# Optimization experiments

Hardware: AMD Instinct MI355X
Metric: run time of the kernel (lower is better)

Reference implementation:

```python
import jax, jax.numpy as jnp
import numpy as np

B = 32768
D_IN = 512      # input_dim == dict_dim (forced by the STE add)
HID = 512       # hard-coded hidden width of linear1
D = 512         # dict_dim / embedding_dim
P = 8           # per_factor_dict_size: number of codebooks / MLP branches
K = 10          # num_factor: codebook size (rows per embedding table)
COMMIT = 0.25


def setup_inputs() -> dict:
    key = jax.random.key(0)
    ks = jax.random.split(key, 7)
    s1 = 1.0 / np.sqrt(D_IN)
    s2 = 1.0 / np.sqrt(HID)
    return {
        "inputs": jax.random.normal(ks[0], (B, D_IN), jnp.float32),
        "W1": jax.random.uniform(ks[1], (P, HID, D_IN), jnp.float32, -s1, s1),
        "b1": jax.random.uniform(ks[2], (P, HID), jnp.float32, -s1, s1),
        "W2": jax.random.uniform(ks[3], (P, D, HID), jnp.float32, -s2, s2),
        "b2": jax.random.uniform(ks[4], (P, D), jnp.float32, -s2, s2),
        # embedding init: uniform(-1/num_factor, 1/num_factor)
        "E": jax.random.uniform(ks[5], (P, K, D), jnp.float32, -1.0 / K, 1.0 / K),
        "label_gen": jax.random.randint(ks[6], (B,), 0, K, jnp.int64),
    }


def reference(inputs, W1, b1, W2, b2, E, label_gen):
    sg = jax.lax.stop_gradient
    # P parallel 2-layer MLPs: [P, B, D]
    h = jax.nn.relu(jnp.einsum("bd,phd->pbh", inputs, W1) + b1[:, None, :])
    z = jnp.einsum("pbh,peh->pbe", h, W2) + b2[:, None, :]
    # squared-distance expansion per codebook: [P, B, K]
    distances = (
        jnp.sum(z * z, axis=-1, keepdims=True)
        + jnp.sum(E * E, axis=-1)[:, None, :]
        - 2.0 * jnp.einsum("pbd,pkd->pbk", z, E)
    )
    ave_distances = jnp.mean(distances, axis=0)          # [B, K]
    idx = jnp.argmin(ave_distances, axis=1)              # [B]
    # one-hot @ E[p] then mean over p == mean codebook gathered at idx
    Emean = jnp.mean(E, axis=0)                          # [K, D]
    vq = Emean[idx]                                      # [B, D]
    vq_z = inputs + sg(vq - inputs)                      # straight-through
    # all_vq_z[j] = mean_p E[p, j]; losses vs every code row: [K, B]
    diff1 = Emean[:, None, :] - sg(inputs)[None, :, :]   # [K, B, D]
    diff2 = sg(Emean)[:, None, :] - inputs[None, :, :]
    all_vq_loss = jnp.sum(diff1 * diff1, axis=-1) + COMMIT * jnp.sum(diff2 * diff2, axis=-1)
    all_vq_z = inputs[None, :, :] + sg(Emean[:, None, :] - inputs[None, :, :])  # [K, B, D]
    changed_vq_z = Emean[label_gen]                      # [B, D]
    return (vq_z, distances, all_vq_z, all_vq_loss, changed_vq_z)
```

## Files before the change

### kernel.cpp

```cpp
#include <hip/hip_runtime.h>
#include <stdint.h>

typedef _Float16 f16;
typedef _Float16 f16x8 __attribute__((ext_vector_type(8)));
typedef float f32x4 __attribute__((ext_vector_type(4)));

#define B_ROWS 32768
#define DIM 512
#define NP 8
#define NK 10

typedef __attribute__((address_space(3))) unsigned int lds_u32;
typedef __attribute__((address_space(1))) const unsigned int gbl_u32;

__device__ __forceinline__ void gload_lds16(const void* g, void* l) {
  __builtin_amdgcn_global_load_lds((gbl_u32*)(uintptr_t)g, (lds_u32*)(uintptr_t)l, 16, 0, 0);
}


__global__ void split_kernel(const float* __restrict__ src, f16* __restrict__ hi,
                             f16* __restrict__ lo, int n) {
  int i = blockIdx.x * 256 + threadIdx.x;
  int stride = gridDim.x * 256;
  for (; i < n; i += stride) {
    float v = src[i];
    f16 h = (f16)v;
    hi[i] = h;
    lo[i] = (f16)(v - (float)h);
  }
}

__global__ void emean_kernel(const float* __restrict__ E, float* __restrict__ Emean) {
  int i = blockIdx.x * 256 + threadIdx.x;
  if (i < NK * DIM) {
    float s = 0.f;
#pragma unroll
    for (int p = 0; p < NP; ++p) s += E[p * NK * DIM + i];
    Emean[i] = s * 0.125f;
  }
}

__global__ void enorm_kernel(const float* __restrict__ E, const float* __restrict__ Emean,
                             float* __restrict__ E2, float* __restrict__ E2m) {
  int bid = blockIdx.x;
  const float* src = (bid < 80) ? (E + (size_t)bid * DIM) : (Emean + (size_t)(bid - 80) * DIM);
  int lane = threadIdx.x;
  float s = 0.f;
  for (int i = lane; i < DIM; i += 64) {
    float v = src[i];
    s = fmaf(v, v, s);
  }
#pragma unroll
  for (int m = 1; m < 64; m <<= 1) s += __shfl_xor(s, m, 64);
  if (lane == 0) {
    if (bid < 80) E2[bid] = s;
    else E2m[bid - 80] = s;
  }
}

__global__ __launch_bounds__(512) void etilde_kernel(const float* __restrict__ W2,
                                                     const float* __restrict__ b2,
                                                     const float* __restrict__ E,
                                                     float* __restrict__ Et,
                                                     float* __restrict__ c_) {
  const int p = blockIdx.x / NK, k = blockIdx.x % NK;
  const int h = threadIdx.x;
  __shared__ float Er[512];
  __shared__ float red[8];
  Er[h] = E[((size_t)p * NK + k) * DIM + h];
  __syncthreads();
  const float* Wp = W2 + (size_t)p * DIM * DIM;
  float s = 0.f;
#pragma unroll 8
  for (int d = 0; d < DIM; ++d) s = fmaf(Wp[(size_t)d * DIM + h], Er[d], s);
  Et[((size_t)p * NK + k) * DIM + h] = s;
  float t = b2[p * DIM + h] * Er[h];
#pragma unroll
  for (int m = 1; m < 64; m <<= 1) t += __shfl_xor(t, m, 64);
  if ((h & 63) == 0) red[h >> 6] = t;
  __syncthreads();
  if (h == 0) {
    float cc = 0.f;
#pragma unroll
    for (int i = 0; i < 8; ++i) cc += red[i];
    c_[p * NK + k] = cc;
  }
}

__global__ void epack_kernel(const float* __restrict__ Et, f16* __restrict__ EimgH,
                             f16* __restrict__ EimgL) {
  int i = blockIdx.x * 256 + threadIdx.x;
  const int tot = NP * 16 * 520;
  if (i >= tot) return;
  int p = i / (16 * 520);
  int rem = i % (16 * 520);
  int k = rem / 520, h = rem % 520;
  float v = (k < NK && h < DIM) ? Et[((size_t)p * NK + k) * DIM + h] : 0.f;
  f16 hi = (f16)v;
  EimgH[i] = hi;
  EimgL[i] = (f16)(v - (float)hi);
}


template <int EPI, int NBN, int NPROD, int GRP>
__global__ __launch_bounds__(256) void gemmA(
    const f16* __restrict__ Ah_, const f16* __restrict__ Al_, int lda, int apitch,
    const f16* __restrict__ Bh_, const f16* __restrict__ Bl_, int bpitch,
    const float* __restrict__ bias_, int bias_pitch,
    f16* __restrict__ Oh, f16* __restrict__ Ol, int ldo,
    float* __restrict__ part2) {
  __shared__ f16 smem[32768];
  const int tid = threadIdx.x;
  const int lane = tid & 63;
  const int wave = tid >> 6;
  const int wr = wave >> 1, wc = wave & 1;
  const int p = blockIdx.z;

  const int q8 = gridDim.x >> 3;
  const int bid = blockIdx.x;
  const int swz = (bid & 7) * q8 + (bid >> 3);
  const int band = swz / (GRP * NBN);
  const int r_ = swz % (GRP * NBN);
  const int bm = band * GRP + (r_ % GRP);
  const int bn = r_ / GRP;
  const int m0 = bm * 128, n0 = bn * 128;

  const f16* Ahp = Ah_ + (size_t)p * apitch;
  const f16* Alp = Al_ + (size_t)p * apitch;
  const f16* Bhp = Bh_ + (size_t)p * bpitch;
  const f16* Blp = Bl_ + (size_t)p * bpitch;

  const int NT = (NPROD == 3) ? 24 : 8;

  f32x4 acc[4][4] = {};

  auto stage = [&](int buf, int t) {
    const f16* As;
    const f16* Bs;
    int k0;
    if (NPROD == 3) {
      int pr = t % 3;
      As = (pr == 2) ? Alp : Ahp;
      Bs = (pr == 1) ? Blp : Bhp;
      k0 = (t / 3) * 64;
    } else {
      As = Ahp;
      Bs = Bhp;
      k0 = t * 64;
    }
    f16* sA = smem + buf * 16384;
    f16* sB = sA + 8192;
#pragma unroll
    for (int j = 0; j < 4; ++j) {
      int r = j * 32 + (tid >> 3);
      int c = ((tid & 7) ^ (r & 7)) * 8;
      gload_lds16(As + (size_t)(m0 + r) * lda + k0 + c, sA + j * 2048 + tid * 8);
      gload_lds16(Bs + (size_t)(n0 + r) * 512 + k0 + c, sB + j * 2048 + tid * 8);
    }
  };

  stage(0, 0);
  __syncthreads();

  const int g = lane >> 4, rl = lane & 15;

  for (int s = 0; s < NT; ++s) {
    int nx = s + 1;
    if (nx < NT) stage(nx & 1, nx);
    const char* sA = (const char*)(smem + (s & 1) * 16384);
    const char* sB = sA + 16384;
    f16x8 af[4][2], bf[4][2];
#pragma unroll
    for (int i = 0; i < 4; ++i) {
      int ra = wr * 64 + i * 16 + rl;
      int rb = wc * 64 + i * 16 + rl;
#pragma unroll
      for (int kk = 0; kk < 2; ++kk) {
        int cb = kk * 64 + g * 16;
        af[i][kk] = *(const f16x8*)(sA + ra * 128 + (cb ^ ((ra & 7) << 4)));
        bf[i][kk] = *(const f16x8*)(sB + rb * 128 + (cb ^ ((rb & 7) << 4)));
      }
    }
#pragma unroll
    for (int i = 0; i < 4; ++i)
#pragma unroll
      for (int jn = 0; jn < 4; ++jn)
#pragma unroll
        for (int kk = 0; kk < 2; ++kk)
          acc[i][jn] = __builtin_amdgcn_mfma_f32_16x16x32_f16(af[i][kk], bf[jn][kk], acc[i][jn], 0, 0, 0);
    __syncthreads();
  }

  if (EPI == 0) {
#pragma unroll
    for (int jn = 0; jn < 4; ++jn) {
      int cg = n0 + wc * 64 + jn * 16 + rl;
      float bv = bias_[cg];
#pragma unroll
      for (int i = 0; i < 4; ++i) {
        int r0 = m0 + wr * 64 + i * 16 + g * 4;
#pragma unroll
        for (int r = 0; r < 4; ++r) {
          float z = acc[i][jn][r] + bv;
          z = fmaxf(z, 0.f);
          f16 h = (f16)z;
          size_t off = (size_t)(r0 + r) * ldo + cg;
          Oh[off] = h;
          Ol[off] = (f16)(z - (float)h);
        }
      }
    }
  } else {
    const float* bp = bias_ + (size_t)p * bias_pitch;
    float bvals[4];
#pragma unroll
    for (int jn = 0; jn < 4; ++jn) bvals[jn] = bp[n0 + wc * 64 + jn * 16 + rl];
    const int ch = bn * 2 + wc;
    float* pb = part2 + (size_t)(p * 8 + ch) * B_ROWS;
#pragma unroll
    for (int i = 0; i < 4; ++i) {
#pragma unroll
      for (int r = 0; r < 4; ++r) {
        float q = 0.f;
#pragma unroll
        for (int jn = 0; jn < 4; ++jn) {
          float z = acc[i][jn][r] + bvals[jn];
          q = fmaf(z, z, q);
        }
#pragma unroll
        for (int m = 1; m < 16; m <<= 1) q += __shfl_xor(q, m, 64);
        if (rl == 0) pb[m0 + wr * 64 + i * 16 + g * 4 + r] = q;
      }
    }
  }
}


__global__ __launch_bounds__(256) void dots_mfma(const f16* __restrict__ Hh,
                                                 const f16* __restrict__ Hl,
                                                 const f16* __restrict__ EimgH,
                                                 const f16* __restrict__ EimgL,
                                                 const float* __restrict__ c_,
                                                 float* __restrict__ gout) {
  __shared__ f16 sH[8192];
  __shared__ f16 sL[8192];
  __shared__ f16 sEh[16 * 520];
  __shared__ f16 sEl[16 * 520];
  const int tid = threadIdx.x;
  const int lane = tid & 63, wave = tid >> 6;
  const int p = blockIdx.y;
  const int r0 = blockIdx.x * 128;
  {
    const uint32_t* ih = (const uint32_t*)(EimgH + (size_t)p * 16 * 520);
    const uint32_t* il = (const uint32_t*)(EimgL + (size_t)p * 16 * 520);
    uint32_t* oh = (uint32_t*)sEh;
    uint32_t* ol = (uint32_t*)sEl;
    for (int i = tid; i < 16 * 520 / 2; i += 256) {
      oh[i] = ih[i];
      ol[i] = il[i];
    }
  }
  const int gq = lane >> 4, rl = lane & 15;
  f32x4 acc[2] = {};
  for (int t = 0; t < 8; ++t) {
    __syncthreads();
#pragma unroll
    for (int j = 0; j < 4; ++j) {
      int r = j * 32 + (tid >> 3);
      int c = ((tid & 7) ^ (r & 7)) * 8;
      gload_lds16(Hh + (size_t)(r0 + r) * 4096 + p * DIM + t * 64 + c, sH + j * 2048 + tid * 8);
      gload_lds16(Hl + (size_t)(r0 + r) * 4096 + p * DIM + t * 64 + c, sL + j * 2048 + tid * 8);
    }
    __syncthreads();
    const char* bh = (const char*)sH;
    const char* bl = (const char*)sL;
    const char* eh = (const char*)sEh;
    const char* el = (const char*)sEl;
    f16x8 ah[2][2], al[2][2], beh[2], bel[2];
#pragma unroll
    for (int mf = 0; mf < 2; ++mf) {
      int ra = wave * 32 + mf * 16 + rl;
#pragma unroll
      for (int kk = 0; kk < 2; ++kk) {
        int cb = kk * 64 + gq * 16;
        ah[mf][kk] = *(const f16x8*)(bh + ra * 128 + (cb ^ ((ra & 7) << 4)));
        al[mf][kk] = *(const f16x8*)(bl + ra * 128 + (cb ^ ((ra & 7) << 4)));
      }
    }
#pragma unroll
    for (int kk = 0; kk < 2; ++kk) {
      int cb = t * 128 + kk * 64 + gq * 16;
      beh[kk] = *(const f16x8*)(eh + rl * 1040 + cb);
      bel[kk] = *(const f16x8*)(el + rl * 1040 + cb);
    }
#pragma unroll
    for (int mf = 0; mf < 2; ++mf)
#pragma unroll
      for (int kk = 0; kk < 2; ++kk) {
        acc[mf] = __builtin_amdgcn_mfma_f32_16x16x32_f16(ah[mf][kk], beh[kk], acc[mf], 0, 0, 0);
        acc[mf] = __builtin_amdgcn_mfma_f32_16x16x32_f16(ah[mf][kk], bel[kk], acc[mf], 0, 0, 0);
        acc[mf] = __builtin_amdgcn_mfma_f32_16x16x32_f16(al[mf][kk], beh[kk], acc[mf], 0, 0, 0);
      }
  }
  if (rl < NK) {
    float cv = c_[p * NK + rl];
#pragma unroll
    for (int mf = 0; mf < 2; ++mf)
#pragma unroll
      for (int r = 0; r < 4; ++r) {
        int row = r0 + wave * 32 + mf * 16 + gq * 4 + r;
        gout[((size_t)p * B_ROWS + row) * NK + rl] = acc[mf][r] + cv;
      }
  }
}


__global__ __launch_bounds__(256) void final_kernel(
    const float* __restrict__ X, const float* __restrict__ part2,
    const float* __restrict__ g, const float* __restrict__ E2,
    const float* __restrict__ Emean, const float* __restrict__ E2m,
    const int* __restrict__ label, float* __restrict__ vq_z,
    float* __restrict__ dist, float* __restrict__ loss, float* __restrict__ changed) {
  __shared__ float Em[NK * DIM];
  __shared__ float e2s[NK];
  for (int i = threadIdx.x; i < NK * DIM; i += 256) Em[i] = Emean[i];
  if (threadIdx.x < NK) e2s[threadIdx.x] = E2m[threadIdx.x];
  __syncthreads();
  const int lane = threadIdx.x & 63, wave = threadIdx.x >> 6;
  const int pl = lane & 7, kh = lane >> 3;
  for (int rr = 0; rr < 4; ++rr) {
    int b = blockIdx.x * 16 + wave * 4 + rr;
    float zq = part2[(size_t)(pl * 8 + kh) * B_ROWS + b];
    zq += __shfl_xor(zq, 8, 64);
    zq += __shfl_xor(zq, 16, 64);
    zq += __shfl_xor(zq, 32, 64);
    float g0 = g[((size_t)pl * B_ROWS + b) * NK + kh];
    float g1 = (lane < 16) ? g[((size_t)pl * B_ROWS + b) * NK + 8 + kh] : 0.f;
    float dv0 = zq + E2[pl * NK + kh] - 2.f * g0;
    float dv1 = zq + E2[pl * NK + 8 + kh] - 2.f * g1;
    dist[((size_t)pl * B_ROWS + b) * NK + kh] = dv0;
    if (lane < 16) dist[((size_t)pl * B_ROWS + b) * NK + 8 + kh] = dv1;
    float v0 = dv0, v1 = dv1;
#pragma unroll
    for (int m = 1; m < 8; m <<= 1) {
      v0 += __shfl_xor(v0, m, 64);
      v1 += __shfl_xor(v1, m, 64);
    }
    float a[NK];
#pragma unroll
    for (int k = 0; k < 8; ++k) a[k] = __shfl(v0, k * 8, 64);
    a[8] = __shfl(v1, 0, 64);
    a[9] = __shfl(v1, 8, 64);
    int idx = 0;
    float mn = a[0];
#pragma unroll
    for (int k = 1; k < NK; ++k) {
      if (a[k] < mn) { mn = a[k]; idx = k; }
    }
    const float* xr = X + (size_t)b * DIM;
    float sx = 0.f, dx[NK] = {};
#pragma unroll
    for (int j = 0; j < 8; ++j) {
      float x = xr[j * 64 + lane];
      sx = fmaf(x, x, sx);
#pragma unroll
      for (int k = 0; k < NK; ++k) dx[k] = fmaf(x, Em[k * DIM + j * 64 + lane], dx[k]);
    }
#pragma unroll
    for (int m = 1; m < 64; m <<= 1) {
      sx += __shfl_xor(sx, m, 64);
#pragma unroll
      for (int k = 0; k < NK; ++k) dx[k] += __shfl_xor(dx[k], m, 64);
    }
    if (lane == 0) {
#pragma unroll
      for (int k = 0; k < NK; ++k)
        loss[(size_t)k * B_ROWS + b] = 1.25f * (sx - 2.f * dx[k] + e2s[k]);
    }
    int lab = label[b];
#pragma unroll
    for (int j = 0; j < 8; ++j) {
      int c = j * 64 + lane;
      vq_z[(size_t)b * DIM + c] = Em[idx * DIM + c];
      changed[(size_t)b * DIM + c] = Em[lab * DIM + c];
    }
  }
}


__global__ void bcast_kernel(const float* __restrict__ Emean, float4* __restrict__ out) {
  const float4* Em4 = (const float4*)Emean;
  size_t n = (size_t)NK * B_ROWS * (DIM / 4);
  for (size_t i = (size_t)blockIdx.x * blockDim.x + threadIdx.x; i < n;
       i += (size_t)gridDim.x * blockDim.x) {
    size_t kb = i >> 7;
    int d4 = (int)(i & 127);
    int k = (int)(kb >> 15);
    out[i] = Em4[k * 128 + d4];
  }
}


extern "C" void kernel_launch(void* const* d_in, const int* in_sizes, int n_in,
                              void* d_out, int out_size, void* d_ws, size_t ws_size,
                              hipStream_t stream) {
  const float* X = (const float*)d_in[0];
  const float* W1 = (const float*)d_in[1];
  const float* b1 = (const float*)d_in[2];
  const float* W2 = (const float*)d_in[3];
  const float* b2 = (const float*)d_in[4];
  const float* E = (const float*)d_in[5];
  const int* lab = (const int*)d_in[6];
  float* out = (float*)d_out;

  float* vq_z = out;
  float* dist = out + 16777216;
  float* avz = out + 16777216 + 2621440;
  float* loss = avz + 167772160;
  float* chg = loss + 327680;

  f16* Xh = (f16*)vq_z;
  f16* Xl = Xh + 16777216;
  f16* Hh = (f16*)avz;
  f16* Hl = Hh + 134217728;
  float* part2 = avz + 134217728;
  float* gbuf = part2 + 2097152;

  char* w = (char*)d_ws;
  f16* W1h = (f16*)w; w += 4194304;
  f16* W1l = (f16*)w; w += 4194304;
  f16* W2h = (f16*)w; w += 4194304;
  f16* W2l = (f16*)w; w += 4194304;
  float* Emean = (float*)w; w += NK * DIM * 4;
  float* E2 = (float*)w; w += 512;
  float* E2m = (float*)w; w += 256;
  float* Et = (float*)w; w += NP * NK * DIM * 4;
  float* c_ = (float*)w; w += 512;
  f16* EimgH = (f16*)w; w += NP * 16 * 520 * 2;
  f16* EimgL = (f16*)w; w += NP * 16 * 520 * 2;

  split_kernel<<<2048, 256, 0, stream>>>(X, Xh, Xl, 16777216);
  split_kernel<<<512, 256, 0, stream>>>(W1, W1h, W1l, 2097152);
  split_kernel<<<512, 256, 0, stream>>>(W2, W2h, W2l, 2097152);
  emean_kernel<<<20, 256, 0, stream>>>(E, Emean);
  enorm_kernel<<<90, 64, 0, stream>>>(E, Emean, E2, E2m);
  etilde_kernel<<<80, 512, 0, stream>>>(W2, b2, E, Et, c_);
  epack_kernel<<<260, 256, 0, stream>>>(Et, EimgH, EimgL);

  gemmA<0, 32, 3, 8><<<dim3(8192, 1, 1), 256, 0, stream>>>(
      Xh, Xl, 512, 0, W1h, W1l, 0, b1, 0, Hh, Hl, 4096, nullptr);
  gemmA<1, 4, 1, 1><<<dim3(1024, 1, NP), 256, 0, stream>>>(
      Hh, Hh, 4096, 512, W2h, W2h, 262144, b2, 512, nullptr, nullptr, 0, part2);

  dots_mfma<<<dim3(256, NP), 256, 0, stream>>>(Hh, Hl, EimgH, EimgL, c_, gbuf);
  final_kernel<<<2048, 256, 0, stream>>>(X, part2, gbuf, E2, Emean, E2m, lab,
                                         vq_z, dist, loss, chg);
  bcast_kernel<<<4096, 256, 0, stream>>>(Emean, (float4*)avz);
}
```

Baseline: 1.140 ms.

## Add 256x256-tile 8-wave GEMM for first layer with quarter-phase LDS pipelining

Adds a new gemm8 kernel with 512 threads, 256x256 output tiles, a 128KB LDS double buffer, and a four-phase schedule that interleaves half-tile async loads with MFMA groups under explicit barriers and priority hints. It replaces the 128-tile gemmA for the first-layer 3-product split-f16 GEMM, aiming to raise data reuse per LDS byte and overlap global loads with compute. It also drops the unused low-part split of W2, saving one conversion pass and workspace, and fixes a masking issue in the final kernel's v1 reduction. The large LDS footprint limits occupancy to one block per CU, and there is risk of register pressure from 32 accumulator vectors per thread.

```diff
diff --git a/kernel.cpp b/kernel.cpp
--- a/kernel.cpp
+++ b/kernel.cpp
@@ -28,6 +28,12 @@
     hi[i] = h;
     lo[i] = (f16)(v - (float)h);
   }
+}
+
+__global__ void splith_kernel(const float* __restrict__ src, f16* __restrict__ hi, int n) {
+  int i = blockIdx.x * 256 + threadIdx.x;
+  int stride = gridDim.x * 256;
+  for (; i < n; i += stride) hi[i] = (f16)src[i];
 }
 
 __global__ void emean_kernel(const float* __restrict__ E, float* __restrict__ Emean) {
@@ -99,6 +105,208 @@
   f16 hi = (f16)v;
   EimgH[i] = hi;
   EimgL[i] = (f16)(v - (float)hi);
+}
+
+
+template <int EPI, int NBN, int NPROD, int GRP>
+__global__ __launch_bounds__(512) void gemm8(
+    const f16* __restrict__ Ah_, const f16* __restrict__ Al_, int lda, int apitch,
+    const f16* __restrict__ Bh_, const f16* __restrict__ Bl_, int bpitch,
+    const float* __restrict__ bias_, int bias_pitch,
+    f16* __restrict__ Oh, f16* __restrict__ Ol, int ldo, float* __restrict__ part2) {
+  __shared__ f16 smem[65536];
+  const int tid = threadIdx.x;
+  const int lane = tid & 63;
+  const int wave = tid >> 6;
+  const int wr = wave >> 2;
+  const int wc = wave & 3;
+  const int g = lane >> 4, rl = lane & 15;
+  const int p = blockIdx.z;
+
+  const int q8 = gridDim.x >> 3;
+  const int bid = blockIdx.x;
+  const int swz = (bid & 7) * q8 + (bid >> 3);
+  const int band = swz / (GRP * NBN);
+  const int r_ = swz % (GRP * NBN);
+  const int bm = band * GRP + (r_ % GRP);
+  const int bn = r_ / GRP;
+  const int m0 = bm * 256, n0 = bn * 256;
+
+  const f16* Ahp = Ah_ + (size_t)p * apitch;
+  const f16* Alp = Al_ + (size_t)p * apitch;
+  const f16* Bhp = Bh_ + (size_t)p * bpitch;
+  const f16* Blp = Bl_ + (size_t)p * bpitch;
+
+  const int NT = (NPROD == 3) ? 24 : 8;
+
+  f32x4 acc[8][4] = {};
+
+  auto stage_half = [&](int t, int ht) {
+    if (t >= NT) return;
+    const f16* As;
+    const f16* Bs;
+    int k0;
+    if (NPROD == 3) {
+      int pr = t % 3;
+      As = (pr == 2) ? Alp : Ahp;
+      Bs = (pr == 1) ? Blp : Bhp;
+      k0 = (t / 3) * 64;
+    } else {
+      As = Ahp;
+      Bs = Bhp;
+      k0 = t * 64;
+    }
+    f16* dst = smem + (t & 1) * 32768 + ht * 8192;
+#pragma unroll
+    for (int rnd = 0; rnd < 2; ++rnd) {
+      int w = rnd * 512 + tid;
+      int row = w >> 3;
+      int col = ((w & 7) ^ (row & 7)) * 8;
+      const f16* src = (ht < 2)
+          ? As + (size_t)(m0 + (ht & 1) * 128 + row) * lda + k0 + col
+          : Bs + (size_t)(n0 + (ht & 1) * 128 + row) * 512 + k0 + col;
+      gload_lds16(src, dst + (size_t)w * 8);
+    }
+  };
+
+  const int ck0 = ((0 * 4 + g) ^ (rl & 7)) << 4;
+  const int ck1 = ((1 * 4 + g) ^ (rl & 7)) << 4;
+  const int abase = wr * 16384 + rl * 128;
+  const int bbase = 32768 + wc * 8192 + rl * 128;
+
+#define SB0 __builtin_amdgcn_sched_barrier(0)
+#define BAR __builtin_amdgcn_s_barrier()
+#define LGKM0 asm volatile("s_waitcnt lgkmcnt(0)" ::: "memory")
+
+  stage_half(0, 0); stage_half(0, 1); stage_half(0, 2); stage_half(0, 3);
+  stage_half(1, 0); stage_half(1, 1);
+  asm volatile("s_waitcnt vmcnt(4)" ::: "memory");
+  BAR;
+
+  for (int t = 0; t < NT; ++t) {
+    const char* sb = (const char*)(smem + (t & 1) * 32768);
+    f16x8 afA[4][2], afB[4][2], bfA[2][2], bfB[2][2];
+
+#pragma unroll
+    for (int i = 0; i < 4; ++i) {
+      afA[i][0] = *(const f16x8*)(sb + abase + i * 2048 + ck0);
+      afA[i][1] = *(const f16x8*)(sb + abase + i * 2048 + ck1);
+    }
+#pragma unroll
+    for (int j = 0; j < 2; ++j) {
+      bfA[j][0] = *(const f16x8*)(sb + bbase + j * 2048 + ck0);
+      bfA[j][1] = *(const f16x8*)(sb + bbase + j * 2048 + ck1);
+    }
+    stage_half(t + 1, 2);
+    SB0; BAR; LGKM0; SB0;
+    __builtin_amdgcn_s_setprio(1);
+#pragma unroll
+    for (int i = 0; i < 4; ++i)
+#pragma unroll
+      for (int j = 0; j < 2; ++j)
+#pragma unroll
+        for (int kk = 0; kk < 2; ++kk)
+          acc[i][j] = __builtin_amdgcn_mfma_f32_16x16x32_f16(afA[i][kk], bfA[j][kk], acc[i][j], 0, 0, 0);
+    __builtin_amdgcn_s_setprio(0);
+    SB0; BAR;
+
+#pragma unroll
+    for (int i = 0; i < 4; ++i) {
+      afB[i][0] = *(const f16x8*)(sb + abase + (i + 4) * 2048 + ck0);
+      afB[i][1] = *(const f16x8*)(sb + abase + (i + 4) * 2048 + ck1);
+    }
+    stage_half(t + 1, 3);
+    SB0; BAR; LGKM0; SB0;
+    __builtin_amdgcn_s_setprio(1);
+#pragma unroll
+    for (int i = 0; i < 4; ++i)
+#pragma unroll
+      for (int j = 0; j < 2; ++j)
+#pragma unroll
+        for (int kk = 0; kk < 2; ++kk)
+          acc[i + 4][j] = __builtin_amdgcn_mfma_f32_16x16x32_f16(afB[i][kk], bfA[j][kk], acc[i + 4][j], 0, 0, 0);
+    __builtin_amdgcn_s_setprio(0);
+    SB0; BAR;
+
+#pragma unroll
+    for (int j = 0; j < 2; ++j) {
+      bfB[j][0] = *(const f16x8*)(sb + bbase + (j + 2) * 2048 + ck0);
+      bfB[j][1] = *(const f16x8*)(sb + bbase + (j + 2) * 2048 + ck1);
+    }
+    stage_half(t + 2, 0);
+    SB0; BAR; LGKM0; SB0;
+    __builtin_amdgcn_s_setprio(1);
+#pragma unroll
+    for (int i = 0; i < 4; ++i)
+#pragma unroll
+      for (int j = 0; j < 2; ++j)
+#pragma unroll
+        for (int kk = 0; kk < 2; ++kk)
+          acc[i][j + 2] = __builtin_amdgcn_mfma_f32_16x16x32_f16(afA[i][kk], bfB[j][kk], acc[i][j + 2], 0, 0, 0);
+    __builtin_amdgcn_s_setprio(0);
+    SB0; BAR;
+
+    stage_half(t + 2, 1);
+    if (t < NT - 2) asm volatile("s_waitcnt vmcnt(4)" ::: "memory");
+    else            asm volatile("s_waitcnt vmcnt(0)" ::: "memory");
+    SB0; BAR;
+    __builtin_amdgcn_s_setprio(1);
+#pragma unroll
+    for (int i = 0; i < 4; ++i)
+#pragma unroll
+      for (int j = 0; j < 2; ++j)
+#pragma unroll
+        for (int kk = 0; kk < 2; ++kk)
+          acc[i + 4][j + 2] = __builtin_amdgcn_mfma_f32_16x16x32_f16(afB[i][kk], bfB[j][kk], acc[i + 4][j + 2], 0, 0, 0);
+    __builtin_amdgcn_s_setprio(0);
+    SB0; BAR;
+  }
+#undef SB0
+#undef BAR
+#undef LGKM0
+
+  if (EPI == 0) {
+#pragma unroll
+    for (int jn = 0; jn < 4; ++jn) {
+      int cg = n0 + wc * 64 + jn * 16 + rl;
+      float bv = bias_[cg];
+#pragma unroll
+      for (int i = 0; i < 8; ++i) {
+#pragma unroll
+        for (int r = 0; r < 4; ++r) {
+          int row = m0 + wr * 128 + i * 16 + g * 4 + r;
+          float z = acc[i][jn][r] + bv;
+          z = fmaxf(z, 0.f);
+          f16 h = (f16)z;
+          size_t off = (size_t)row * ldo + cg;
+          Oh[off] = h;
+          Ol[off] = (f16)(z - (float)h);
+        }
+      }
+    }
+  } else {
+    const float* bp = bias_ + (size_t)p * bias_pitch;
+    float bvals[4];
+#pragma unroll
+    for (int jn = 0; jn < 4; ++jn) bvals[jn] = bp[n0 + wc * 64 + jn * 16 + rl];
+    const int ch = bn * 4 + wc;
+    float* pb = part2 + (size_t)(p * 8 + ch) * B_ROWS;
+#pragma unroll
+    for (int i = 0; i < 8; ++i) {
+#pragma unroll
+      for (int r = 0; r < 4; ++r) {
+        float q = 0.f;
+#pragma unroll
+        for (int jn = 0; jn < 4; ++jn) {
+          float z = acc[i][jn][r] + bvals[jn];
+          q = fmaf(z, z, q);
+        }
+#pragma unroll
+        for (int m = 1; m < 16; m <<= 1) q += __shfl_xor(q, m, 64);
+        if (rl == 0) pb[m0 + wr * 128 + i * 16 + g * 4 + r] = q;
+      }
+    }
+  }
 }
 
 
@@ -340,7 +548,7 @@
     float dv1 = zq + E2[pl * NK + 8 + kh] - 2.f * g1;
     dist[((size_t)pl * B_ROWS + b) * NK + kh] = dv0;
     if (lane < 16) dist[((size_t)pl * B_ROWS + b) * NK + 8 + kh] = dv1;
-    float v0 = dv0, v1 = dv1;
+    float v0 = dv0, v1 = (lane < 16) ? dv1 : 0.f;
 #pragma unroll
     for (int m = 1; m < 8; m <<= 1) {
       v0 += __shfl_xor(v0, m, 64);
@@ -430,7 +638,6 @@
   f16* W1h = (f16*)w; w += 4194304;
   f16* W1l = (f16*)w; w += 4194304;
   f16* W2h = (f16*)w; w += 4194304;
-  f16* W2l = (f16*)w; w += 4194304;
   float* Emean = (float*)w; w += NK * DIM * 4;
   float* E2 = (float*)w; w += 512;
   float* E2m = (float*)w; w += 256;
@@ -441,13 +648,13 @@
 
   split_kernel<<<2048, 256, 0, stream>>>(X, Xh, Xl, 16777216);
   split_kernel<<<512, 256, 0, stream>>>(W1, W1h, W1l, 2097152);
-  split_kernel<<<512, 256, 0, stream>>>(W2, W2h, W2l, 2097152);
+  splith_kernel<<<512, 256, 0, stream>>>(W2, W2h, 2097152);
   emean_kernel<<<20, 256, 0, stream>>>(E, Emean);
   enorm_kernel<<<90, 64, 0, stream>>>(E, Emean, E2, E2m);
   etilde_kernel<<<80, 512, 0, stream>>>(W2, b2, E, Et, c_);
   epack_kernel<<<260, 256, 0, stream>>>(Et, EimgH, EimgL);
 
-  gemmA<0, 32, 3, 8><<<dim3(8192, 1, 1), 256, 0, stream>>>(
+  gemm8<0, 16, 3, 4><<<dim3(2048, 1, 1), 512, 0, stream>>>(
       Xh, Xl, 512, 0, W1h, W1l, 0, b1, 0, Hh, Hl, 4096, nullptr);
   gemmA<1, 4, 1, 1><<<dim3(1024, 1, NP), 256, 0, stream>>>(
       Hh, Hh, 4096, 512, W2h, W2h, 262144, b2, 512, nullptr, nullptr, 0, part2);
```

New measurement: 1.211 ms. 6.2% more time.

## Fuse prep kernels and fold the all_vq_z broadcast into the final kernel

Applied to the files above, without the earlier changes.

The X/W1/W2 split kernels become one launch, and W2 no longer gets a low-half split. Emean and its norms are computed in one kernel, and etilde writes the padded fp16 hi/lo image directly, so the epack kernel and the Et buffer go away. dots_mfma now writes straight into the dist output, which final_kernel updates in place instead of going through a scratch buffer. final_kernel also writes most of the all_vq_z broadcast while Emean sits in shared memory. The slab that overlaps still-live scratch (part2) is left to a small trailing kernel, cutting launches and redundant traffic, with careful aliasing needed to keep writes ordered.

```diff
diff --git a/kernel.cpp b/kernel.cpp
--- a/kernel.cpp
+++ b/kernel.cpp
@@ -18,50 +18,70 @@
 }
 
 
-__global__ void split_kernel(const float* __restrict__ src, f16* __restrict__ hi,
-                             f16* __restrict__ lo, int n) {
-  int i = blockIdx.x * 256 + threadIdx.x;
-  int stride = gridDim.x * 256;
-  for (; i < n; i += stride) {
-    float v = src[i];
-    f16 h = (f16)v;
-    hi[i] = h;
-    lo[i] = (f16)(v - (float)h);
-  }
-}
-
-__global__ void emean_kernel(const float* __restrict__ E, float* __restrict__ Emean) {
-  int i = blockIdx.x * 256 + threadIdx.x;
-  if (i < NK * DIM) {
+__global__ void prep_split(const float* __restrict__ X, f16* __restrict__ Xh,
+                           f16* __restrict__ Xl, const float* __restrict__ W1,
+                           f16* __restrict__ W1h, f16* __restrict__ W1l,
+                           const float* __restrict__ W2, f16* __restrict__ W2h) {
+  int bid = blockIdx.x, tid = threadIdx.x;
+  if (bid < 2048) {
+    for (int i = bid * 256 + tid; i < 16777216; i += 2048 * 256) {
+      float v = X[i];
+      f16 h = (f16)v;
+      Xh[i] = h;
+      Xl[i] = (f16)(v - (float)h);
+    }
+  } else if (bid < 2560) {
+    for (int i = (bid - 2048) * 256 + tid; i < 2097152; i += 512 * 256) {
+      float v = W1[i];
+      f16 h = (f16)v;
+      W1h[i] = h;
+      W1l[i] = (f16)(v - (float)h);
+    }
+  } else {
+    for (int i = (bid - 2560) * 256 + tid; i < 2097152; i += 512 * 256) {
+      W2h[i] = (f16)W2[i];
+    }
+  }
+}
+
+
+__global__ void enorm2(const float* __restrict__ E, float* __restrict__ Emean,
+                       float* __restrict__ E2, float* __restrict__ E2m) {
+  int bid = blockIdx.x;
+  int lane = threadIdx.x;
+  if (bid < 80) {
+    const float* src = E + (size_t)bid * DIM;
     float s = 0.f;
-#pragma unroll
-    for (int p = 0; p < NP; ++p) s += E[p * NK * DIM + i];
-    Emean[i] = s * 0.125f;
-  }
-}
-
-__global__ void enorm_kernel(const float* __restrict__ E, const float* __restrict__ Emean,
-                             float* __restrict__ E2, float* __restrict__ E2m) {
-  int bid = blockIdx.x;
-  const float* src = (bid < 80) ? (E + (size_t)bid * DIM) : (Emean + (size_t)(bid - 80) * DIM);
-  int lane = threadIdx.x;
-  float s = 0.f;
-  for (int i = lane; i < DIM; i += 64) {
-    float v = src[i];
-    s = fmaf(v, v, s);
-  }
-#pragma unroll
-  for (int m = 1; m < 64; m <<= 1) s += __shfl_xor(s, m, 64);
-  if (lane == 0) {
-    if (bid < 80) E2[bid] = s;
-    else E2m[bid - 80] = s;
-  }
-}
+    for (int i = lane; i < DIM; i += 64) {
+      float v = src[i];
+      s = fmaf(v, v, s);
+    }
+#pragma unroll
+    for (int m = 1; m < 64; m <<= 1) s += __shfl_xor(s, m, 64);
+    if (lane == 0) E2[bid] = s;
+  } else {
+    int k = bid - 80;
+    float acc = 0.f;
+    for (int i = lane; i < DIM; i += 64) {
+      float s = 0.f;
+#pragma unroll
+      for (int p = 0; p < NP; ++p) s += E[p * NK * DIM + k * DIM + i];
+      s *= 0.125f;
+      Emean[k * DIM + i] = s;
+      acc = fmaf(s, s, acc);
+    }
+#pragma unroll
+    for (int m = 1; m < 64; m <<= 1) acc += __shfl_xor(acc, m, 64);
+    if (lane == 0) E2m[k] = acc;
+  }
+}
+
 
 __global__ __launch_bounds__(512) void etilde_kernel(const float* __restrict__ W2,
                                                      const float* __restrict__ b2,
                                                      const float* __restrict__ E,
-                                                     float* __restrict__ Et,
+                                                     f16* __restrict__ EimgH,
+                                                     f16* __restrict__ EimgL,
                                                      float* __restrict__ c_) {
   const int p = blockIdx.x / NK, k = blockIdx.x % NK;
   const int h = threadIdx.x;
@@ -73,7 +93,22 @@
   float s = 0.f;
 #pragma unroll 8
   for (int d = 0; d < DIM; ++d) s = fmaf(Wp[(size_t)d * DIM + h], Er[d], s);
-  Et[((size_t)p * NK + k) * DIM + h] = s;
+  int ei = p * 8320 + k * 520 + h;
+  f16 hi = (f16)s;
+  EimgH[ei] = hi;
+  EimgL[ei] = (f16)(s - (float)hi);
+  if (h < 8) {
+    int pi = p * 8320 + k * 520 + 512 + h;
+    EimgH[pi] = (f16)0.f;
+    EimgL[pi] = (f16)0.f;
+  }
+  if (k == 0) {
+    for (int j = h; j < 6 * 520; j += 512) {
+      int pi = p * 8320 + 10 * 520 + j;
+      EimgH[pi] = (f16)0.f;
+      EimgL[pi] = (f16)0.f;
+    }
+  }
   float t = b2[p * DIM + h] * Er[h];
 #pragma unroll
   for (int m = 1; m < 64; m <<= 1) t += __shfl_xor(t, m, 64);
@@ -85,20 +120,6 @@
     for (int i = 0; i < 8; ++i) cc += red[i];
     c_[p * NK + k] = cc;
   }
-}
-
-__global__ void epack_kernel(const float* __restrict__ Et, f16* __restrict__ EimgH,
-                             f16* __restrict__ EimgL) {
-  int i = blockIdx.x * 256 + threadIdx.x;
-  const int tot = NP * 16 * 520;
-  if (i >= tot) return;
-  int p = i / (16 * 520);
-  int rem = i % (16 * 520);
-  int k = rem / 520, h = rem % 520;
-  float v = (k < NK && h < DIM) ? Et[((size_t)p * NK + k) * DIM + h] : 0.f;
-  f16 hi = (f16)v;
-  EimgH[i] = hi;
-  EimgL[i] = (f16)(v - (float)hi);
 }
 
 
@@ -317,30 +338,52 @@
 
 __global__ __launch_bounds__(256) void final_kernel(
     const float* __restrict__ X, const float* __restrict__ part2,
-    const float* __restrict__ g, const float* __restrict__ E2,
+    float* __restrict__ gdist, const float* __restrict__ E2,
     const float* __restrict__ Emean, const float* __restrict__ E2m,
     const int* __restrict__ label, float* __restrict__ vq_z,
-    float* __restrict__ dist, float* __restrict__ loss, float* __restrict__ changed) {
+    float* __restrict__ avz, float* __restrict__ loss, float* __restrict__ changed) {
   __shared__ float Em[NK * DIM];
   __shared__ float e2s[NK];
-  for (int i = threadIdx.x; i < NK * DIM; i += 256) Em[i] = Emean[i];
-  if (threadIdx.x < NK) e2s[threadIdx.x] = E2m[threadIdx.x];
+  const int tid = threadIdx.x;
+  for (int i = tid; i < NK * DIM; i += 256) Em[i] = Emean[i];
+  if (tid < NK) e2s[tid] = E2m[tid];
   __syncthreads();
-  const int lane = threadIdx.x & 63, wave = threadIdx.x >> 6;
+
+  const int b0 = blockIdx.x * 16;
+  {
+    const float4* Em4 = (const float4*)Em;
+    float4* avz4 = (float4*)avz;
+    if (blockIdx.x < 256) {
+      for (int it = 0; it < 80; ++it) {
+        int idx = it * 256 + tid;
+        int d4 = idx & 127, row = (idx >> 7) & 15, k = idx >> 11;
+        if (k == 8) continue;
+        avz4[(((size_t)k * B_ROWS + b0 + row) << 7) + d4] = Em4[k * 128 + d4];
+      }
+    } else {
+      for (int it = 0; it < 80; ++it) {
+        int idx = it * 256 + tid;
+        int d4 = idx & 127, row = (idx >> 7) & 15, k = idx >> 11;
+        avz4[(((size_t)k * B_ROWS + b0 + row) << 7) + d4] = Em4[k * 128 + d4];
+      }
+    }
+  }
+
+  const int lane = tid & 63, wave = tid >> 6;
   const int pl = lane & 7, kh = lane >> 3;
   for (int rr = 0; rr < 4; ++rr) {
-    int b = blockIdx.x * 16 + wave * 4 + rr;
+    int b = b0 + wave * 4 + rr;
     float zq = part2[(size_t)(pl * 8 + kh) * B_ROWS + b];
     zq += __shfl_xor(zq, 8, 64);
     zq += __shfl_xor(zq, 16, 64);
     zq += __shfl_xor(zq, 32, 64);
-    float g0 = g[((size_t)pl * B_ROWS + b) * NK + kh];
-    float g1 = (lane < 16) ? g[((size_t)pl * B_ROWS + b) * NK + 8 + kh] : 0.f;
+    float g0 = gdist[((size_t)pl * B_ROWS + b) * NK + kh];
+    float g1 = (lane < 16) ? gdist[((size_t)pl * B_ROWS + b) * NK + 8 + kh] : 0.f;
     float dv0 = zq + E2[pl * NK + kh] - 2.f * g0;
     float dv1 = zq + E2[pl * NK + 8 + kh] - 2.f * g1;
-    dist[((size_t)pl * B_ROWS + b) * NK + kh] = dv0;
-    if (lane < 16) dist[((size_t)pl * B_ROWS + b) * NK + 8 + kh] = dv1;
-    float v0 = dv0, v1 = dv1;
+    gdist[((size_t)pl * B_ROWS + b) * NK + kh] = dv0;
+    if (lane < 16) gdist[((size_t)pl * B_ROWS + b) * NK + 8 + kh] = dv1;
+    float v0 = dv0, v1 = (lane < 16) ? dv1 : 0.f;
 #pragma unroll
     for (int m = 1; m < 8; m <<= 1) {
       v0 += __shfl_xor(v0, m, 64);
@@ -388,15 +431,13 @@
 }
 
 
-__global__ void bcast_kernel(const float* __restrict__ Emean, float4* __restrict__ out) {
+__global__ void bcast_rest(const float* __restrict__ Emean, float4* __restrict__ avz4) {
   const float4* Em4 = (const float4*)Emean;
-  size_t n = (size_t)NK * B_ROWS * (DIM / 4);
-  for (size_t i = (size_t)blockIdx.x * blockDim.x + threadIdx.x; i < n;
-       i += (size_t)gridDim.x * blockDim.x) {
-    size_t kb = i >> 7;
-    int d4 = (int)(i & 127);
-    int k = (int)(kb >> 15);
-    out[i] = Em4[k * 128 + d4];
+  int tid = blockIdx.x * 256 + threadIdx.x;
+  for (int it = 0; it < 32; ++it) {
+    int idx = tid + it * 16384;
+    int b = idx >> 7, d4 = idx & 127;
+    avz4[((size_t)(8 * B_ROWS + b) << 7) + d4] = Em4[8 * 128 + d4];
   }
 }
 
@@ -424,36 +465,29 @@
   f16* Hh = (f16*)avz;
   f16* Hl = Hh + 134217728;
   float* part2 = avz + 134217728;
-  float* gbuf = part2 + 2097152;
 
   char* w = (char*)d_ws;
   f16* W1h = (f16*)w; w += 4194304;
   f16* W1l = (f16*)w; w += 4194304;
   f16* W2h = (f16*)w; w += 4194304;
-  f16* W2l = (f16*)w; w += 4194304;
   float* Emean = (float*)w; w += NK * DIM * 4;
   float* E2 = (float*)w; w += 512;
   float* E2m = (float*)w; w += 256;
-  float* Et = (float*)w; w += NP * NK * DIM * 4;
   float* c_ = (float*)w; w += 512;
   f16* EimgH = (f16*)w; w += NP * 16 * 520 * 2;
   f16* EimgL = (f16*)w; w += NP * 16 * 520 * 2;
 
-  split_kernel<<<2048, 256, 0, stream>>>(X, Xh, Xl, 16777216);
-  split_kernel<<<512, 256, 0, stream>>>(W1, W1h, W1l, 2097152);
-  split_kernel<<<512, 256, 0, stream>>>(W2, W2h, W2l, 2097152);
-  emean_kernel<<<20, 256, 0, stream>>>(E, Emean);
-  enorm_kernel<<<90, 64, 0, stream>>>(E, Emean, E2, E2m);
-  etilde_kernel<<<80, 512, 0, stream>>>(W2, b2, E, Et, c_);
-  epack_kernel<<<260, 256, 0, stream>>>(Et, EimgH, EimgL);
+  prep_split<<<3072, 256, 0, stream>>>(X, Xh, Xl, W1, W1h, W1l, W2, W2h);
+  enorm2<<<90, 64, 0, stream>>>(E, Emean, E2, E2m);
+  etilde_kernel<<<80, 512, 0, stream>>>(W2, b2, E, EimgH, EimgL, c_);
 
   gemmA<0, 32, 3, 8><<<dim3(8192, 1, 1), 256, 0, stream>>>(
       Xh, Xl, 512, 0, W1h, W1l, 0, b1, 0, Hh, Hl, 4096, nullptr);
   gemmA<1, 4, 1, 1><<<dim3(1024, 1, NP), 256, 0, stream>>>(
       Hh, Hh, 4096, 512, W2h, W2h, 262144, b2, 512, nullptr, nullptr, 0, part2);
 
-  dots_mfma<<<dim3(256, NP), 256, 0, stream>>>(Hh, Hl, EimgH, EimgL, c_, gbuf);
-  final_kernel<<<2048, 256, 0, stream>>>(X, part2, gbuf, E2, Emean, E2m, lab,
-                                         vq_z, dist, loss, chg);
-  bcast_kernel<<<4096, 256, 0, stream>>>(Emean, (float4*)avz);
-}
+  dots_mfma<<<dim3(256, NP), 256, 0, stream>>>(Hh, Hl, EimgH, EimgL, c_, dist);
+  final_kernel<<<2048, 256, 0, stream>>>(X, part2, dist, E2, Emean, E2m, lab,
+                                         vq_z, avz, loss, chg);
+  bcast_rest<<<64, 256, 0, stream>>>(Emean, (float4*)avz);
+}
```

Result: faster. 1.100 ms (-3.5%).
